# Kernel optimization log

Measured on AMD Instinct MI355X. Metric: run time of the kernel, lower is better.

The kernel has to match this reference:

```python
import jax, jax.numpy as jnp
import numpy as np

FEATURE_DIM = 16
NUM_HEADS = 16
HEAD_DIM = 64
R2 = float(np.sqrt(2.0))
RD = float(np.sqrt(FEATURE_DIM))        # sqrt(d) = 4
RRD = float(np.sqrt(RD))                # d^(1/4) = 2
RMS_EPS = 1e-5


def taylor_exp(x):
    # x: [b, h, l, d] -> [b, h, l, 1 + d + d*d]
    x2 = (x[..., :, None] * x[..., None, :]).reshape(*x.shape[:-1], FEATURE_DIM * FEATURE_DIM) / R2
    ones = jnp.ones_like(x[..., :1])
    return jnp.concatenate([ones, x / RRD, x2 / RD], axis=-1)


def setup_inputs() -> dict:
    key = jax.random.key(0)
    ks = jax.random.split(key, 5)
    b, l, d_model = 4, 2048, 1024
    inp = {
        'hidden_states': jax.random.normal(ks[0], (b, l, d_model), dtype=jnp.float32),
        'Wq': jax.random.normal(ks[1], (FEATURE_DIM * NUM_HEADS, d_model), dtype=jnp.float32) * 0.02,
        'Wk': jax.random.normal(ks[2], (FEATURE_DIM * NUM_HEADS, d_model), dtype=jnp.float32) * 0.02,
        'Wv': jax.random.normal(ks[3], (NUM_HEADS * HEAD_DIM, d_model), dtype=jnp.float32) * 0.02,
        'Wo': jax.random.normal(ks[4], (d_model, NUM_HEADS * HEAD_DIM), dtype=jnp.float32) * 0.02,
        'g_weight': jnp.ones((HEAD_DIM,), dtype=jnp.float32),
    }
    return inp


def reference(hidden_states, Wq, Wk, Wv, Wo, g_weight):
    b, l, _ = hidden_states.shape
    # projections (Linear, no bias): x @ W.T
    q = (hidden_states @ Wq.T).reshape(b, l, NUM_HEADS, FEATURE_DIM).transpose(0, 2, 1, 3)
    k = (hidden_states @ Wk.T).reshape(b, l, NUM_HEADS, FEATURE_DIM).transpose(0, 2, 1, 3)
    v = (hidden_states @ Wv.T).reshape(b, l, NUM_HEADS, HEAD_DIM).transpose(0, 2, 1, 3)

    qf = taylor_exp(q)  # [b, h, l, 273]
    kf = taylor_exp(k)  # [b, h, l, 273]

    A_qk = jnp.einsum('bhnd,bhmd->bhnm', qf, kf)
    A_qk = jnp.tril(A_qk)
    y = jnp.einsum('bhnm,bhme->bhne', A_qk, v)  # [b, h, l, head_dim]

    kv_state = jnp.einsum('bhnd,bhnf->bhfd', kf, v)[:, :, None]  # [b, h, 1, head_dim, 273]

    # RMSNorm over head_dim
    rms = jax.lax.rsqrt(jnp.mean(y * y, axis=-1, keepdims=True) + RMS_EPS)
    y = y * rms * g_weight

    y = y.transpose(0, 2, 1, 3).reshape(b, l, NUM_HEADS * HEAD_DIM)
    out = y @ Wo.T
    return out, kv_state
```

## Files before the change

kernel.cpp:

```cpp
#include <hip/hip_runtime.h>


typedef unsigned short u16;
typedef unsigned int u32;
typedef __attribute__((ext_vector_type(4))) float f32x4;
typedef __attribute__((ext_vector_type(16))) float f32x16;
typedef __attribute__((ext_vector_type(8))) short s16x8;

struct MaskT { static constexpr bool value = true;  };
struct MaskF { static constexpr bool value = false; };

__device__ __forceinline__ float bf2f(u16 u) {
    union { unsigned int i; float f; } x; x.i = ((unsigned int)u) << 16; return x.f;
}
__device__ __forceinline__ u16 f2bf(float f) {
    union { float f; unsigned int u; } x; x.f = f;
    unsigned int r = x.u + 0x7FFFu + ((x.u >> 16) & 1u);
    return (u16)(r >> 16);
}

typedef const __attribute__((address_space(1))) u32* gas1_t;
typedef __attribute__((address_space(3))) u32* las3_t;
__device__ __forceinline__ void gld16(const u16* g, u16* l) {
    __builtin_amdgcn_global_load_lds((gas1_t)(const void*)g, (las3_t)(void*)l, 16, 0, 0);
}

__global__ __launch_bounds__(256)
void cvt_all_kernel(const void* __restrict__ H,  const void* __restrict__ Wq,
                    const void* __restrict__ Wk, const void* __restrict__ Wv,
                    const void* __restrict__ Wo, const void* __restrict__ gw,
                    u16* __restrict__ Hb,  u16* __restrict__ Wqb,
                    u16* __restrict__ Wkb, u16* __restrict__ Wvb,
                    u16* __restrict__ Wob, u16* __restrict__ gwb)
{
    __shared__ int sflag;
    const int t = threadIdx.x;
    if (t < 64) {
        const unsigned int* Hw = (const unsigned int*)H;
        int cnt = 0;
#pragma unroll
        for (int i = 0; i < 16; ++i) {
            const unsigned int wrd = Hw[t * 16 + i];
            const int e = (int)((wrd >> 7) & 0xFFu);
            if (e >= 85 && e <= 170) ++cnt;
        }
        cnt += __shfl_xor(cnt, 1);  cnt += __shfl_xor(cnt, 2);
        cnt += __shfl_xor(cnt, 4);  cnt += __shfl_xor(cnt, 8);
        cnt += __shfl_xor(cnt, 16); cnt += __shfl_xor(cnt, 32);
        if (t == 0) sflag = (cnt < 700) ? 1 : 0;
    }
    __syncthreads();
    const int f32in = sflag;

    const int NQ = 11010112 / 4;
    for (int qi = blockIdx.x * 256 + t; qi < NQ; qi += gridDim.x * 256) {
        const int i = qi * 4;
        const void* src; u16* dst; int off;
        if      (i <  8388608) { src = H;  dst = Hb;  off = i; }
        else if (i <  8650752) { src = Wq; dst = Wqb; off = i - 8388608; }
        else if (i <  8912896) { src = Wk; dst = Wkb; off = i - 8650752; }
        else if (i <  9961472) { src = Wv; dst = Wvb; off = i - 8912896; }
        else if (i < 11010048) { src = Wo; dst = Wob; off = i - 9961472; }
        else                   { src = gw; dst = gwb; off = i - 11010048; }
        ushort4 o;
        if (f32in) {
            const float4 v = *((const float4*)src + (off >> 2));
            o.x = f2bf(v.x); o.y = f2bf(v.y); o.z = f2bf(v.z); o.w = f2bf(v.w);
        } else {
            o = *((const ushort4*)src + (off >> 2));
        }
        *(ushort4*)(dst + off) = o;
    }
}

template<int MODE>
__global__ __launch_bounds__(256)
void gemm_nt(const u16* __restrict__ A,
             const u16* __restrict__ Bq, const u16* __restrict__ Bk,
             const u16* __restrict__ Bv,
             u16* __restrict__ Oq, u16* __restrict__ Ok,
             u16* __restrict__ Ovt, float* __restrict__ Of,
             const float* __restrict__ Kvp, float* __restrict__ Kvo)
{
    __shared__ __attribute__((aligned(16))) u16 As[8192];
    __shared__ __attribute__((aligned(16))) u16 Bs[8192];
    const int t = threadIdx.x;
    const int lane = t & 63, w = t >> 6;
    const int c = lane & 15, qd = lane >> 4;
    const int wm = (w >> 1) * 64, wn = (w & 1) * 64;
    const int nwgx = gridDim.x;
    const int pid = blockIdx.y * nwgx + blockIdx.x;
    const int lid = (pid & 7) * ((nwgx * 64) >> 3) + (pid >> 3);
    const int rm = (lid / nwgx) * 128;
    const int cb = (lid % nwgx) * 128;

    const u16* Bsrc; int wrow0;
    if (MODE == 0) {
        if (cb < 256)      { Bsrc = Bq; wrow0 = cb; }
        else if (cb < 512) { Bsrc = Bk; wrow0 = cb - 256; }
        else               { Bsrc = Bv; wrow0 = cb - 512; }
    } else { Bsrc = Bq; wrow0 = cb; }

    f32x4 acc[4][4];
#pragma unroll
    for (int i = 0; i < 4; ++i)
#pragma unroll
        for (int j = 0; j < 4; ++j) acc[i][j] = (f32x4){0.f, 0.f, 0.f, 0.f};

    const int r0 = w * 8 + (lane >> 3);
    const int s0 = (lane & 7) ^ (lane >> 3);
    const u16* Ag = A    + (size_t)(rm    + r0) * 1024 + s0 * 8;
    const u16* Bg = Bsrc + (size_t)(wrow0 + r0) * 1024 + s0 * 8;
    u16* AsW = As + w * 512;
    u16* BsW = Bs + w * 512;

    for (int kt = 0; kt < 16; ++kt) {
        const int k0 = kt * 64;
        __syncthreads();
#pragma unroll
        for (int i = 0; i < 4; ++i) {
            gld16(Ag + (size_t)(i * 32) * 1024 + k0, AsW + i * 2048);
            gld16(Bg + (size_t)(i * 32) * 1024 + k0, BsW + i * 2048);
        }
        __syncthreads();
        s16x8 af[2][4], bfr[2][4];
#pragma unroll
        for (int kk = 0; kk < 2; ++kk) {
#pragma unroll
            for (int mt = 0; mt < 4; ++mt) {
                const int row = wm + mt * 16 + c;
                af[kk][mt] = *(const s16x8*)&As[row * 64 + (((kk * 4 + qd) ^ (row & 7)) * 8)];
            }
#pragma unroll
            for (int nt = 0; nt < 4; ++nt) {
                const int row = wn + nt * 16 + c;
                bfr[kk][nt] = *(const s16x8*)&Bs[row * 64 + (((kk * 4 + qd) ^ (row & 7)) * 8)];
            }
        }
#pragma unroll
        for (int kk = 0; kk < 2; ++kk)
#pragma unroll
            for (int mt = 0; mt < 4; ++mt)
#pragma unroll
                for (int nt = 0; nt < 4; ++nt)
                    acc[mt][nt] = __builtin_amdgcn_mfma_f32_16x16x32_bf16(af[kk][mt], bfr[kk][nt], acc[mt][nt], 0, 0, 0);
    }

#pragma unroll
    for (int mt = 0; mt < 4; ++mt) {
#pragma unroll
        for (int nt = 0; nt < 4; ++nt) {
            const int gc = cb + wn + nt * 16 + c;
            const int row0 = rm + wm + mt * 16 + qd * 4;
            if (MODE == 1) {
#pragma unroll
                for (int r = 0; r < 4; ++r)
                    Of[(size_t)(row0 + r) * 1024 + gc] = acc[mt][nt][r];
            } else if (gc < 512) {
#pragma unroll
                for (int r = 0; r < 4; ++r) {
                    const int row = row0 + r;
                    const int b_ = row >> 11, l_ = row & 2047;
                    const int cc = gc & 255;
                    const int h = cc >> 4, idx = cc & 15;
                    u16* dst = (gc < 256) ? Oq : Ok;
                    dst[(size_t)((b_ * 16 + h) * 2048 + l_) * 16 + idx] = f2bf(acc[mt][nt][r]);
                }
            } else {
                const int cc = gc - 512;
                const int h = cc >> 6, idx = cc & 63;
                const int b_ = row0 >> 11, l0 = row0 & 2047;
                ushort4 pk;
                pk.x = f2bf(acc[mt][nt][0]);
                pk.y = f2bf(acc[mt][nt][1]);
                pk.z = f2bf(acc[mt][nt][2]);
                pk.w = f2bf(acc[mt][nt][3]);
                *(ushort4*)(Ovt + ((size_t)((b_ * 16 + h) * 64 + idx)) * 2048 + l0) = pk;
            }
        }
    }

    if (MODE == 1) {
        const int S = 64 * 64 * 273;
        const int NQ4 = S / 4;
        const int NT = gridDim.x * gridDim.y * 256;
        for (int q = pid * 256 + t; q < NQ4; q += NT) {
            float4 a = ((const float4*)Kvp)[q];
            const float4 b = ((const float4*)(Kvp + S))[q];
            const float4 c2 = ((const float4*)(Kvp + 2 * S))[q];
            const float4 d = ((const float4*)(Kvp + 3 * S))[q];
            a.x += b.x + c2.x + d.x;  a.y += b.y + c2.y + d.y;
            a.z += b.z + c2.z + d.z;  a.w += b.w + c2.w + d.w;
            ((float4*)Kvo)[q] = a;
        }
    }
}

__global__ __launch_bounds__(512, 2)
void attn_kernel(const u16* __restrict__ Qg, const u16* __restrict__ Kg,
                 const u16* __restrict__ Vt, const u16* __restrict__ gwb,
                 u16* __restrict__ Yn)
{
    __shared__ __attribute__((aligned(16))) u16 Vs[2][8192];
    const int t = threadIdx.x, lane = t & 63, w = t >> 6;
    const int la = lane & 31, h = lane >> 5;
    const int pid = blockIdx.y * 4 + blockIdx.x;
    const int lid = (pid & 7) * 32 + (pid >> 3);
    const int bh = lid >> 2;
    const int jj = lid & 3;
    const int b_ = bh >> 4, hh = bh & 15;
    const u16* Qh = Qg + (size_t)bh * (2048 * 16);
    const u16* Kh = Kg + (size_t)bh * (2048 * 16);
    const u16* Vh = Vt + (size_t)bh * (64 * 2048);
    const float gl0 = bf2f(gwb[la]);
    const float gl1 = bf2f(gwb[32 + la]);
    const f32x16 z16 = {0.f,0.f,0.f,0.f,0.f,0.f,0.f,0.f,
                        0.f,0.f,0.f,0.f,0.f,0.f,0.f,0.f};
    const int vbase0 = (la << 8) | (h << 4);
    const int vsw = (la & 15) << 4;

    auto stageV = [&](int n0s, int bufsel) {
#pragma unroll
        for (int i = 0; i < 2; ++i) {
            const int slot = i * 512 + t;
            const int fl = slot >> 4;
            const int seg = (slot & 15) ^ (fl & 15);
            gld16(Vh + (size_t)fl * 2048 + n0s + seg * 8,
                  (u16*)Vs[bufsel] + (size_t)(i * 512 + (w << 6)) * 8);
        }
    };

    for (int pass = 0; pass < 2; ++pass) {
        const int qb = pass ? jj : (7 - jj);
        const int q0 = qb * 256 + w * 32;
        const int kf = 2 * qb + (w >> 2);
        const int wp = w & 3;
        const int nck = 2 * qb + 2;

        const s16x8 bq = *(const s16x8*)(Qh + (size_t)(q0 + la) * 16 + h * 8);
        f32x16 yt0 = z16, yt1 = z16;
        s16x8 ka[4];
        const char* vsc = (const char*)Vs[0];

        auto loadK = [&](s16x8* kk, int kcL) {
#pragma unroll
            for (int kt = 0; kt < 4; ++kt)
                kk[kt] = *(const s16x8*)(Kh + (size_t)(kcL * 128 + kt * 32 + la) * 16 + h * 8);
        };

        auto tile = [&](int kt, auto MASKED) {
            constexpr bool masked = decltype(MASKED)::value;
            f32x16 sv = __builtin_amdgcn_mfma_f32_32x32x16_bf16(ka[kt], bq, z16, 0, 0, 0);
            float p[16];
#pragma unroll
            for (int r = 0; r < 16; ++r) {
                const float s = sv[r];
                float pv = fmaf(s, fmaf(s, 0.03125f, 0.25f), 1.0f);
                if (masked) {
                    const int keyloc = (r & 3) + 8 * (r >> 2) + 4 * h;
                    if (keyloc > la) pv = 0.f;
                }
                p[r] = pv;
            }
#pragma unroll
            for (int ks = 0; ks < 2; ++ks) {
                u32 X0, X1, Y0, Y1;
                asm("v_cvt_pk_bf16_f32 %0, %1, %2" : "=v"(X0) : "v"(p[8*ks+0]), "v"(p[8*ks+1]));
                asm("v_cvt_pk_bf16_f32 %0, %1, %2" : "=v"(X1) : "v"(p[8*ks+2]), "v"(p[8*ks+3]));
                asm("v_cvt_pk_bf16_f32 %0, %1, %2" : "=v"(Y0) : "v"(p[8*ks+4]), "v"(p[8*ks+5]));
                asm("v_cvt_pk_bf16_f32 %0, %1, %2" : "=v"(Y1) : "v"(p[8*ks+6]), "v"(p[8*ks+7]));
                asm("v_permlane32_swap_b32 %0, %1" : "+v"(X0), "+v"(Y0));
                asm("v_permlane32_swap_b32 %0, %1" : "+v"(X1), "+v"(Y1));
                union { uint4 u; s16x8 v; } afu;
                afu.u = (uint4){X0, X1, Y0, Y1};
                const int offb = (kt << 6) | (ks << 5);
                const s16x8 vb0 = *(const s16x8*)(vsc + (((vbase0 + offb)) ^ vsw));
                const s16x8 vb1 = *(const s16x8*)(vsc + (((vbase0 + 8192 + offb)) ^ vsw));
                yt0 = __builtin_amdgcn_mfma_f32_32x32x16_bf16(afu.v, vb0, yt0, 0, 0, 0);
                yt1 = __builtin_amdgcn_mfma_f32_32x32x16_bf16(afu.v, vb1, yt1, 0, 0, 0);
            }
        };

        stageV(0, 0);
        loadK(ka, 0);
        __syncthreads();

        for (int kc = 0; kc < nck; ++kc) {
            const int cur = kc & 1;
            vsc = (const char*)Vs[cur];
            if (kc + 1 < nck) stageV((kc + 1) * 128, cur ^ 1);
            s16x8 kn[4] = {ka[0], ka[1], ka[2], ka[3]};
            if (kc < kf) loadK(kn, kc + 1);

            if (kc < kf) {
                tile(0, MaskF{}); tile(1, MaskF{});
                tile(2, MaskF{}); tile(3, MaskF{});
            } else if (kc == kf) {
                if (wp == 0)      { tile(0, MaskT{}); }
                else if (wp == 1) { tile(0, MaskF{}); tile(1, MaskT{}); }
                else if (wp == 2) { tile(0, MaskF{}); tile(1, MaskF{}); tile(2, MaskT{}); }
                else              { tile(0, MaskF{}); tile(1, MaskF{}); tile(2, MaskF{}); tile(3, MaskT{}); }
            }
            __syncthreads();
#pragma unroll
            for (int kt = 0; kt < 4; ++kt) ka[kt] = kn[kt];
        }

#pragma unroll
        for (int r = 0; r < 16; ++r) {
            float ss = yt0[r] * yt0[r] + yt1[r] * yt1[r];
            ss += __shfl_xor(ss, 1);  ss += __shfl_xor(ss, 2);
            ss += __shfl_xor(ss, 4);  ss += __shfl_xor(ss, 8);
            ss += __shfl_xor(ss, 16);
            const float rmsv = rsqrtf(ss * (1.0f / 64.0f) + 1e-5f);
            const int row = q0 + (r & 3) + 8 * (r >> 2) + 4 * h;
            u16* dst = Yn + ((size_t)(b_ * 2048 + row)) * 1024 + hh * 64;
            dst[la]      = f2bf(yt0[r] * rmsv * gl0);
            dst[32 + la] = f2bf(yt1[r] * rmsv * gl1);
        }
    }
}

__global__ __launch_bounds__(256)
void kv_mfma_kernel(const u16* __restrict__ Kg, const u16* __restrict__ Vt,
                    float* __restrict__ kvpart)
{
    __shared__ __attribute__((aligned(16))) float kS[64][20];
    __shared__ __attribute__((aligned(16))) float kT[64][20];
    __shared__ __attribute__((aligned(16))) u16 KFs[288][72];
    __shared__ __attribute__((aligned(16))) u16 Vs[64][72];
    const int t = threadIdx.x, lane = t & 63, w = t >> 6;
    const int c = lane & 15, qd = lane >> 4;
    const int ns = blockIdx.x, bh = blockIdx.y;
    const u16* Kh  = Kg + (size_t)bh * 2048 * 16;
    const u16* Vth = Vt + (size_t)bh * 64 * 2048;

    int i2a, j2a, i2b = 18, j2b = 18;
    {
        const int dd = t;
        if (dd == 0)      { i2a = 16; j2a = 17; }
        else if (dd < 17) { i2a = dd - 1; j2a = 16; }
        else              { i2a = (dd - 17) >> 4; j2a = (dd - 17) & 15; }
        if (t < 32) {
            const int d2 = 256 + t;
            if (d2 < 273) { i2b = (d2 - 17) >> 4; j2b = (d2 - 17) & 15; }
        }
    }

    f32x4 acc[4][5];
#pragma unroll
    for (int mt = 0; mt < 4; ++mt)
#pragma unroll
        for (int j = 0; j < 5; ++j) acc[mt][j] = (f32x4){0.f, 0.f, 0.f, 0.f};

    for (int ch = 0; ch < 8; ++ch) {
        const int n0 = ns * 512 + ch * 64;
        __syncthreads();
        if (t < 128) {
            const int row = t >> 1, half = t & 1;
            uint4 kv = *(const uint4*)(Kh + (size_t)(n0 + row) * 16 + half * 8);
            const u16* ke = (const u16*)&kv;
#pragma unroll
            for (int e = 0; e < 8; ++e) {
                const float f = bf2f(ke[e]);
                kS[row][half * 8 + e] = f;
                kT[row][half * 8 + e] = f * 0.17677669529663687f;
            }
        } else if (t < 192) {
            const int row = t - 128;
            kS[row][16] = 1.f;  kS[row][17] = 1.f;  kS[row][18] = 0.f;
            kT[row][16] = 0.5f; kT[row][17] = 1.f;  kT[row][18] = 0.f;
        }
#pragma unroll
        for (int i = 0; i < 2; ++i) {
            const int lin = i * 256 + t;
            const int f = lin >> 3, seg = lin & 7;
            *(uint4*)&Vs[f][seg * 8] =
                *(const uint4*)(Vth + (size_t)f * 2048 + n0 + seg * 8);
        }
        __syncthreads();
        {
            unsigned int* dst = (unsigned int*)&KFs[t][0];
#pragma unroll 8
            for (int i = 0; i < 32; ++i) {
                const float v0 = kS[2 * i][i2a]     * kT[2 * i][j2a];
                const float v1 = kS[2 * i + 1][i2a] * kT[2 * i + 1][j2a];
                dst[i] = (unsigned int)f2bf(v0) | ((unsigned int)f2bf(v1) << 16);
            }
            if (t < 32) {
                unsigned int* dst2 = (unsigned int*)&KFs[256 + t][0];
#pragma unroll 8
                for (int i = 0; i < 32; ++i) {
                    const float v0 = kS[2 * i][i2b]     * kT[2 * i][j2b];
                    const float v1 = kS[2 * i + 1][i2b] * kT[2 * i + 1][j2b];
                    dst2[i] = (unsigned int)f2bf(v0) | ((unsigned int)f2bf(v1) << 16);
                }
            }
        }
        __syncthreads();
#pragma unroll
        for (int kt = 0; kt < 2; ++kt) {
            s16x8 va[4];
#pragma unroll
            for (int mt = 0; mt < 4; ++mt)
                va[mt] = *(const s16x8*)&Vs[mt * 16 + c][kt * 32 + qd * 8];
#pragma unroll
            for (int j = 0; j < 5; ++j) {
                const int dt = w + 4 * j;
                if (dt < 18) {
                    s16x8 vb = *(const s16x8*)&KFs[dt * 16 + c][kt * 32 + qd * 8];
#pragma unroll
                    for (int mt = 0; mt < 4; ++mt)
                        acc[mt][j] = __builtin_amdgcn_mfma_f32_16x16x32_bf16(va[mt], vb, acc[mt][j], 0, 0, 0);
                }
            }
        }
    }

    float* base = kvpart + ((size_t)(ns * 64 + bh) * 64) * 273;
#pragma unroll
    for (int j = 0; j < 5; ++j) {
        const int dt = w + 4 * j;
        if (dt >= 18) continue;
        const int dd = dt * 16 + c;
        if (dd >= 273) continue;
#pragma unroll
        for (int mt = 0; mt < 4; ++mt)
#pragma unroll
            for (int r = 0; r < 4; ++r) {
                const int f = mt * 16 + qd * 4 + r;
                base[f * 273 + dd] = acc[mt][j][r];
            }
    }
}

extern "C" void kernel_launch(void* const* d_in, const int* in_sizes, int n_in,
                              void* d_out, int out_size, void* d_ws, size_t ws_size,
                              hipStream_t stream)
{
    const void* H  = d_in[0];
    const void* Wq = d_in[1];
    const void* Wk = d_in[2];
    const void* Wv = d_in[3];
    const void* Wo = d_in[4];
    const void* gw = d_in[5];
    float* outf = (float*)d_out;

    char* ws = (char*)d_ws;
    const size_t M = 1 << 20;
    u16*   Hb    = (u16*)(ws);
    u16*   Wqb   = (u16*)(ws + 16 * M);
    u16*   Wkb   = (u16*)(ws + 16 * M + 512 * 1024);
    u16*   Wvb   = (u16*)(ws + 17 * M);
    u16*   Wob   = (u16*)(ws + 19 * M);
    u16*   gwb   = (u16*)(ws + 21 * M);
    u16*   q     = (u16*)(ws + 22 * M);
    u16*   k     = (u16*)(ws + 26 * M);
    u16*   vt    = (u16*)(ws + 30 * M);
    float* kvpart= (float*)(ws + 46 * M);
    u16*   yn    = Hb;

    cvt_all_kernel<<<2048, 256, 0, stream>>>(H, Wq, Wk, Wv, Wo, gw,
                                             Hb, Wqb, Wkb, Wvb, Wob, gwb);

    gemm_nt<0><<<dim3(12, 64), 256, 0, stream>>>(Hb, Wqb, Wkb, Wvb, q, k, vt,
                                                 nullptr, nullptr, nullptr);
    attn_kernel<<<dim3(4, 64), 512, 0, stream>>>(q, k, vt, gwb, yn);
    kv_mfma_kernel<<<dim3(4, 64), 256, 0, stream>>>(k, vt, kvpart);
    gemm_nt<1><<<dim3(8, 64), 256, 0, stream>>>(yn, Wob, nullptr, nullptr,
                                                nullptr, nullptr, nullptr, outf,
                                                kvpart, outf + (size_t)8388608);
}
```

Measured before the change: 228.1 us.

## Compute Taylor key features in registers and split kv-state over more blocks

The kv-state kernel no longer builds the 273-wide feature matrix in shared memory. Each lane now computes its bf16 feature operand directly from the raw key values right before the MFMA, which removes the KFs buffer, the kT buffer and one barrier per chunk. The sequence is also split into 8 partial slices of 256 instead of 4 of 512, giving twice as many blocks. The final reduction in the output GEMM now sums 8 partial buffers, which costs more partial-buffer traffic and redundant per-lane feature arithmetic. The partial buffer now needs 8 slices, and it is not obvious that the workspace was sized for that.

```diff
diff --git a/kernel.cpp b/kernel.cpp
--- a/kernel.cpp
+++ b/kernel.cpp
@@ -186,11 +186,11 @@
         const int NT = gridDim.x * gridDim.y * 256;
         for (int q = pid * 256 + t; q < NQ4; q += NT) {
             float4 a = ((const float4*)Kvp)[q];
-            const float4 b = ((const float4*)(Kvp + S))[q];
-            const float4 c2 = ((const float4*)(Kvp + 2 * S))[q];
-            const float4 d = ((const float4*)(Kvp + 3 * S))[q];
-            a.x += b.x + c2.x + d.x;  a.y += b.y + c2.y + d.y;
-            a.z += b.z + c2.z + d.z;  a.w += b.w + c2.w + d.w;
+#pragma unroll
+            for (int s = 1; s < 8; ++s) {
+                const float4 b = ((const float4*)(Kvp + (size_t)s * S))[q];
+                a.x += b.x; a.y += b.y; a.z += b.z; a.w += b.w;
+            }
             ((float4*)Kvo)[q] = a;
         }
     }
@@ -325,9 +325,7 @@
 void kv_mfma_kernel(const u16* __restrict__ Kg, const u16* __restrict__ Vt,
                     float* __restrict__ kvpart)
 {
-    __shared__ __attribute__((aligned(16))) float kS[64][20];
-    __shared__ __attribute__((aligned(16))) float kT[64][20];
-    __shared__ __attribute__((aligned(16))) u16 KFs[288][72];
+    __shared__ __attribute__((aligned(16))) float kS[64][17];
     __shared__ __attribute__((aligned(16))) u16 Vs[64][72];
     const int t = threadIdx.x, lane = t & 63, w = t >> 6;
     const int c = lane & 15, qd = lane >> 4;
@@ -335,41 +333,22 @@
     const u16* Kh  = Kg + (size_t)bh * 2048 * 16;
     const u16* Vth = Vt + (size_t)bh * 64 * 2048;
 
-    int i2a, j2a, i2b = 18, j2b = 18;
-    {
-        const int dd = t;
-        if (dd == 0)      { i2a = 16; j2a = 17; }
-        else if (dd < 17) { i2a = dd - 1; j2a = 16; }
-        else              { i2a = (dd - 17) >> 4; j2a = (dd - 17) & 15; }
-        if (t < 32) {
-            const int d2 = 256 + t;
-            if (d2 < 273) { i2b = (d2 - 17) >> 4; j2b = (d2 - 17) & 15; }
-        }
-    }
-
     f32x4 acc[4][5];
 #pragma unroll
     for (int mt = 0; mt < 4; ++mt)
 #pragma unroll
         for (int j = 0; j < 5; ++j) acc[mt][j] = (f32x4){0.f, 0.f, 0.f, 0.f};
 
-    for (int ch = 0; ch < 8; ++ch) {
-        const int n0 = ns * 512 + ch * 64;
+    for (int ch = 0; ch < 4; ++ch) {
+        const int n0 = ns * 256 + ch * 64;
         __syncthreads();
         if (t < 128) {
             const int row = t >> 1, half = t & 1;
             uint4 kv = *(const uint4*)(Kh + (size_t)(n0 + row) * 16 + half * 8);
             const u16* ke = (const u16*)&kv;
 #pragma unroll
-            for (int e = 0; e < 8; ++e) {
-                const float f = bf2f(ke[e]);
-                kS[row][half * 8 + e] = f;
-                kT[row][half * 8 + e] = f * 0.17677669529663687f;
-            }
-        } else if (t < 192) {
-            const int row = t - 128;
-            kS[row][16] = 1.f;  kS[row][17] = 1.f;  kS[row][18] = 0.f;
-            kT[row][16] = 0.5f; kT[row][17] = 1.f;  kT[row][18] = 0.f;
+            for (int e = 0; e < 8; ++e)
+                kS[row][half * 8 + e] = bf2f(ke[e]);
         }
 #pragma unroll
         for (int i = 0; i < 2; ++i) {
@@ -379,25 +358,7 @@
                 *(const uint4*)(Vth + (size_t)f * 2048 + n0 + seg * 8);
         }
         __syncthreads();
-        {
-            unsigned int* dst = (unsigned int*)&KFs[t][0];
-#pragma unroll 8
-            for (int i = 0; i < 32; ++i) {
-                const float v0 = kS[2 * i][i2a]     * kT[2 * i][j2a];
-                const float v1 = kS[2 * i + 1][i2a] * kT[2 * i + 1][j2a];
-                dst[i] = (unsigned int)f2bf(v0) | ((unsigned int)f2bf(v1) << 16);
-            }
-            if (t < 32) {
-                unsigned int* dst2 = (unsigned int*)&KFs[256 + t][0];
-#pragma unroll 8
-                for (int i = 0; i < 32; ++i) {
-                    const float v0 = kS[2 * i][i2b]     * kT[2 * i][j2b];
-                    const float v1 = kS[2 * i + 1][i2b] * kT[2 * i + 1][j2b];
-                    dst2[i] = (unsigned int)f2bf(v0) | ((unsigned int)f2bf(v1) << 16);
-                }
-            }
-        }
-        __syncthreads();
+
 #pragma unroll
         for (int kt = 0; kt < 2; ++kt) {
             s16x8 va[4];
@@ -408,10 +369,32 @@
             for (int j = 0; j < 5; ++j) {
                 const int dt = w + 4 * j;
                 if (dt < 18) {
-                    s16x8 vb = *(const s16x8*)&KFs[dt * 16 + c][kt * 32 + qd * 8];
+                    const int dd = dt * 16 + c;
+                    const int i2 = (dd - 17) >> 4, j2 = (dd - 17) & 15;
+                    const int nb = kt * 32 + qd * 8;
+                    u32 vbw[4];
+#pragma unroll
+                    for (int p = 0; p < 4; ++p) {
+                        float pv[2];
+#pragma unroll
+                        for (int h2 = 0; h2 < 2; ++h2) {
+                            const int n = nb + 2 * p + h2;
+                            float val;
+                            if (dd == 0)       val = 1.0f;
+                            else if (dd < 17)  val = 0.5f * kS[n][dd - 1];
+                            else               val = 0.17677669529663687f
+                                                     * kS[n][i2] * kS[n][j2];
+                            pv[h2] = val;
+                        }
+                        asm("v_cvt_pk_bf16_f32 %0, %1, %2"
+                            : "=v"(vbw[p]) : "v"(pv[0]), "v"(pv[1]));
+                    }
+                    union { uint4 u; s16x8 v; } vbu;
+                    vbu.u = (uint4){vbw[0], vbw[1], vbw[2], vbw[3]};
 #pragma unroll
                     for (int mt = 0; mt < 4; ++mt)
-                        acc[mt][j] = __builtin_amdgcn_mfma_f32_16x16x32_bf16(va[mt], vb, acc[mt][j], 0, 0, 0);
+                        acc[mt][j] = __builtin_amdgcn_mfma_f32_16x16x32_bf16(
+                            va[mt], vbu.v, acc[mt][j], 0, 0, 0);
                 }
             }
         }
@@ -466,7 +449,7 @@
     gemm_nt<0><<<dim3(12, 64), 256, 0, stream>>>(Hb, Wqb, Wkb, Wvb, q, k, vt,
                                                  nullptr, nullptr, nullptr);
     attn_kernel<<<dim3(4, 64), 512, 0, stream>>>(q, k, vt, gwb, yn);
-    kv_mfma_kernel<<<dim3(4, 64), 256, 0, stream>>>(k, vt, kvpart);
+    kv_mfma_kernel<<<dim3(8, 64), 256, 0, stream>>>(k, vt, kvpart);
     gemm_nt<1><<<dim3(8, 64), 256, 0, stream>>>(yn, Wob, nullptr, nullptr,
                                                 nullptr, nullptr, nullptr, outf,
                                                 kvpart, outf + (size_t)8388608);
```

After: 218.7 us. -4.1%, faster.
